# Optimization experiments

Measured on AMD Instinct MI355X. Metric: run time of the kernel, lower is better.

## Reference

```python
import jax, jax.numpy as jnp
import numpy as np
import math

TWO_PI = 2.0 * math.pi
B, K, DIM = 8, 1024, 4096
TEMP = 10.0  # softmax temperature from `sims * 10`


def setup_inputs() -> dict:
    key = jax.random.key(0)
    k1, k2 = jax.random.split(key)
    superposed = jax.random.uniform(k1, (B, DIM), jnp.float32, 0.0, TWO_PI)
    codebook = jax.random.uniform(k2, (K, DIM), jnp.float32, 0.0, TWO_PI)
    return {"superposed": superposed, "codebook": codebook, "num_iterations": 50}


def _cos_sim(est, codebook):
    # est: (B, dim), codebook: (K, dim) -> (B, K) mean cosine of phase diff
    return jnp.cos(est[:, None, :] - codebook[None, :, :]).mean(axis=-1)


def reference(superposed, codebook, num_iterations):
    # Batched resonator decode: iteratively refine estimate toward codebook
    # entries via softmax-weighted phasor superposition (torch.angle == atan2).
    cb_cos = jnp.cos(codebook)  # (K, dim) real part of codebook phasors
    cb_sin = jnp.sin(codebook)  # (K, dim) imag part

    def step(est, _):
        sims = _cos_sim(est, codebook)                 # (B, K)
        w = jax.nn.softmax(sims * TEMP, axis=-1)       # (B, K)
        re = w @ cb_cos                                # (B, dim)
        im = w @ cb_sin                                # (B, dim)
        est_new = jnp.arctan2(im, re) % TWO_PI         # angle of complex sum
        return est_new, None

    est, _ = jax.lax.scan(step, superposed, None, length=num_iterations)
    return _cos_sim(est, codebook)  # (B, K) final similarity scores
```

## Files before the change

### kernel.cpp

```cpp
#include <hip/hip_runtime.h>
#include <math.h>


#define KCODES 1024
#define DIMS   4096
#define BATCH  8
#define JROWS  (DIMS * 2)
#define NITER_MAX 50

#define T1_SZF  (JROWS * KCODES / 2)
#define T2_OFF  (T1_SZF)
#define T2_SZF  (T1_SZF)
#define EST_OFF (T2_OFF + T2_SZF)
#define EST_SZ  (JROWS * BATCH)
#define W_OFF   (EST_OFF + EST_SZ)

#define C2 (0.00244140625f * 1.4426950408889634f)

__device__ __forceinline__ ushort f2bf(float x) {
  unsigned u = __float_as_uint(x);
  return (ushort)((u + 0x7FFFu + ((u >> 16) & 1u)) >> 16);
}
__device__ __forceinline__ float bf2f(ushort u) {
  return __uint_as_float(((unsigned)u) << 16);
}

template <int CTRL>
__device__ __forceinline__ float dpp_add(float x) {
  int v = __builtin_amdgcn_update_dpp(0, __float_as_int(x), CTRL, 0xF, 0xF, false);
  return x + __int_as_float(v);
}
__device__ __forceinline__ float wave_sum64(float x) {
  x = dpp_add<0x111>(x);
  x = dpp_add<0x112>(x);
  x = dpp_add<0x114>(x);
  x = dpp_add<0x118>(x);
  x = dpp_add<0x142>(x);
  x = dpp_add<0x143>(x);
  return x;
}

__global__ __launch_bounds__(256) void k_trig(const float* __restrict__ cb,
                                              float* __restrict__ ws) {
  __shared__ float lc[64][65], ls[64][65];
  const int t  = threadIdx.x;
  const int bk = blockIdx.x & 15;
  const int bd = blockIdx.x >> 4;
  const int k0 = bk * 64, d0 = bd * 64;
  const int c = t & 63;
  #pragma unroll
  for (int i = 0; i < 16; ++i) {
    const int r = (t >> 6) + i * 4;
    float a = cb[(size_t)(k0 + r) * DIMS + d0 + c];
    float s, cc; sincosf(a, &s, &cc);
    lc[r][c] = cc; ls[r][c] = s;
  }
  __syncthreads();
  ushort* T1 = (ushort*)ws;
  #pragma unroll
  for (int j = 0; j < 16; ++j) {
    const int dd = (t >> 6) + j * 4;
    T1[(size_t)((d0 + dd) * 2 + 0) * KCODES + k0 + c] = f2bf(lc[c][dd]);
    T1[(size_t)((d0 + dd) * 2 + 1) * KCODES + k0 + c] = f2bf(ls[c][dd]);
  }
}

__global__ __launch_bounds__(256) void k_trig2(const float* __restrict__ cb,
                                               float* __restrict__ ws) {
  __shared__ float cbl[4][DIMS];
  const int t = threadIdx.x;
  const int g = blockIdx.x;
  #pragma unroll
  for (int c = 0; c < 4; ++c)
    #pragma unroll
    for (int q = 0; q < 4; ++q) {
      const int off = (q * 256 + t) * 4;
      *(float4*)&cbl[c][off] = *(const float4*)&cb[(size_t)(4 * g + c) * DIMS + off];
    }
  __syncthreads();

  ushort buf[128];
  #pragma unroll
  for (int dl = 0; dl < 16; ++dl) {
    #pragma unroll
    for (int c = 0; c < 4; ++c) {
      float s, cc; sincosf(cbl[c][16 * t + dl], &s, &cc);
      buf[(2 * dl + 0) * 4 + c] = f2bf(cc);
      buf[(2 * dl + 1) * 4 + c] = f2bf(s);
    }
  }
  uint4* dst = (uint4*)((ushort*)(ws + T2_OFF) + (size_t)g * (JROWS * 4) + t * 128);
  const uint4* src = (const uint4*)buf;
  #pragma unroll
  for (int i = 0; i < 16; ++i) dst[i] = src[i];
}

__global__ __launch_bounds__(256) void k_init(const float* __restrict__ sup,
                                              float* __restrict__ ws) {
  float* EST = ws + EST_OFF;
  const int i = blockIdx.x * 256 + threadIdx.x;
  const int b = i >> 12, d = i & 4095;
  float s, c; sincosf(sup[(size_t)b * DIMS + d], &s, &c);
  EST[(2 * d + 0) * BATCH + b] = c;
  EST[(2 * d + 1) * BATCH + b] = s;
}

__global__ __launch_bounds__(512) void k_simw(float* __restrict__ ws,
                                              const int* __restrict__ nit_p,
                                              float* __restrict__ out,
                                              int it) {
  const int NI = *nit_p;
  if (it > NI) return;
  const ushort* T2  = (const ushort*)(ws + T2_OFF);
  const float*  EST = ws + EST_OFF;
  float* W = ws + W_OFF;
  __shared__ float scr[8 * 32];

  const int t = threadIdx.x, lane = t & 63, wv = t >> 6;
  const int g = blockIdx.x;
  const ushort* trow = T2 + (size_t)g * (JROWS * 4);

  float acc[4][BATCH];
  #pragma unroll
  for (int c = 0; c < 4; ++c)
    #pragma unroll
    for (int b = 0; b < BATCH; ++b) acc[c][b] = 0.f;

  #pragma unroll 4
  for (int i = 0; i < 16; ++i) {
    const int j = i * 512 + t;
    const float4 e0 = *(const float4*)&EST[j * BATCH + 0];
    const float4 e1 = *(const float4*)&EST[j * BATCH + 4];
    const float ev[8] = {e0.x, e0.y, e0.z, e0.w, e1.x, e1.y, e1.z, e1.w};
    const ushort4 tu = *(const ushort4*)&trow[j * 4];
    const float tc[4] = {bf2f(tu.x), bf2f(tu.y), bf2f(tu.z), bf2f(tu.w)};
    #pragma unroll
    for (int c = 0; c < 4; ++c)
      #pragma unroll
      for (int b = 0; b < BATCH; ++b)
        acc[c][b] = fmaf(tc[c], ev[b], acc[c][b]);
  }

  #pragma unroll
  for (int c = 0; c < 4; ++c)
    #pragma unroll
    for (int b = 0; b < BATCH; ++b) {
      const float s = wave_sum64(acc[c][b]);
      if (lane == 63) scr[wv * 32 + c * BATCH + b] = s;
    }
  __syncthreads();

  if (t < 32) {
    float s = 0.f;
    #pragma unroll
    for (int w8 = 0; w8 < 8; ++w8) s += scr[w8 * 32 + t];
    const int c = t >> 3, b = t & 7;
    if (it == NI) out[b * KCODES + 4 * g + c] = s * (1.0f / (float)DIMS);
    else          W[b * KCODES + 4 * g + c] = exp2f(s * C2);
  }
}

__global__ __launch_bounds__(512) void k_est(float* __restrict__ ws,
                                             const int* __restrict__ nit_p,
                                             int it) {
  if (it >= *nit_p) return;
  const ushort* T1 = (const ushort*)ws;
  const float*  Wg = ws + W_OFF;
  float* EST = ws + EST_OFF;

  __shared__ float Wl[BATCH * KCODES];
  __shared__ float est_l[32 * BATCH];

  const int t = threadIdx.x, lane = t & 63, wv = t >> 6;
  const int r0 = blockIdx.x * 32;

  #pragma unroll
  for (int j = 0; j < 4; ++j) {
    const int idx = (j * 512 + t) * 4;
    *(float4*)&Wl[idx] = *(const float4*)&Wg[idx];
  }
  __syncthreads();

  const int rw = wv * 4;
  float acc[4][BATCH];
  #pragma unroll
  for (int r = 0; r < 4; ++r)
    #pragma unroll
    for (int b = 0; b < BATCH; ++b) acc[r][b] = 0.f;

  #pragma unroll
  for (int c = 0; c < 4; ++c) {
    const int kk = c * 256 + lane * 4;
    float4 wr[BATCH];
    #pragma unroll
    for (int b = 0; b < BATCH; ++b)
      wr[b] = *(const float4*)&Wl[b * KCODES + kk];
    #pragma unroll
    for (int r = 0; r < 4; ++r) {
      const ushort4 tu = *(const ushort4*)&T1[(size_t)(r0 + rw + r) * KCODES + kk];
      const float4 tv = make_float4(bf2f(tu.x), bf2f(tu.y), bf2f(tu.z), bf2f(tu.w));
      #pragma unroll
      for (int b = 0; b < BATCH; ++b) {
        acc[r][b] = fmaf(wr[b].x, tv.x, acc[r][b]);
        acc[r][b] = fmaf(wr[b].y, tv.y, acc[r][b]);
        acc[r][b] = fmaf(wr[b].z, tv.z, acc[r][b]);
        acc[r][b] = fmaf(wr[b].w, tv.w, acc[r][b]);
      }
    }
  }
  #pragma unroll
  for (int r = 0; r < 4; ++r)
    #pragma unroll
    for (int b = 0; b < BATCH; ++b) {
      const float s = wave_sum64(acc[r][b]);
      if (lane == 63) est_l[(rw + r) * BATCH + b] = s;
    }
  __syncthreads();

  if (t < 128) {
    const int dl = t >> 3, b = t & 7;
    const float re = est_l[(2 * dl + 0) * BATCH + b];
    const float im = est_l[(2 * dl + 1) * BATCH + b];
    const float n2 = fmaf(re, re, im * im);
    float ec, es;
    if (n2 > 0.f) {
      const float inv = rsqrtf(n2);
      ec = re * inv; es = im * inv;
    } else { ec = 1.f; es = 0.f; }
    est_l[(2 * dl + 0) * BATCH + b] = ec;
    est_l[(2 * dl + 1) * BATCH + b] = es;
  }
  __syncthreads();

  if (t < 256) EST[r0 * BATCH + t] = est_l[t];
}

extern "C" void kernel_launch(void* const* d_in, const int* in_sizes, int n_in,
                              void* d_out, int out_size, void* d_ws, size_t ws_size,
                              hipStream_t stream) {
  const float* sup = (const float*)d_in[0];
  const float* cbk = (const float*)d_in[1];
  const int*   nit = (const int*)d_in[2];
  float* outp = (float*)d_out;
  float* ws   = (float*)d_ws;

  hipLaunchKernelGGL(k_trig,  dim3(1024), dim3(256), 0, stream, cbk, ws);
  hipLaunchKernelGGL(k_trig2, dim3(256),  dim3(256), 0, stream, cbk, ws);
  hipLaunchKernelGGL(k_init,  dim3(128),  dim3(256), 0, stream, sup, ws);

  for (int it = 0; it < NITER_MAX; ++it) {
    hipLaunchKernelGGL(k_simw, dim3(256), dim3(512), 0, stream, ws, nit, outp, it);
    hipLaunchKernelGGL(k_est,  dim3(256), dim3(512), 0, stream, ws, nit, it);
  }
  hipLaunchKernelGGL(k_simw, dim3(256), dim3(512), 0, stream, ws, nit, outp, NITER_MAX);
}
```

Baseline: 765.3 us.

## Fuse similarity and estimate kernels into one launch per iteration with atomic flags

Merges the per-iteration similarity/softmax kernel and the estimate-update kernel into a single 512-block launch. The first 256 blocks compute weights and signal completion through hierarchical atomic counters. The remaining 256 blocks spin on a flag before reading the weights. This halves the kernel launch count and removes the inter-kernel gap. It relies on all 512 blocks being co-resident or being scheduled in order, and it adds a flag-buffer memset plus per-iteration weight buffers.

```diff
diff --git a/kernel.cpp b/kernel.cpp
--- a/kernel.cpp
+++ b/kernel.cpp
@@ -8,12 +8,20 @@
 #define JROWS  (DIMS * 2)
 #define NITER_MAX 50
 
-#define T1_SZF  (JROWS * KCODES / 2)
-#define T2_OFF  (T1_SZF)
-#define T2_SZF  (T1_SZF)
-#define EST_OFF (T2_OFF + T2_SZF)
-#define EST_SZ  (JROWS * BATCH)
-#define W_OFF   (EST_OFF + EST_SZ)
+#define T1_SZF   (JROWS * KCODES / 2)
+#define T2_OFF   (T1_SZF)
+#define T2_SZF   (T1_SZF)
+#define EST_OFF  (T2_OFF + T2_SZF)
+#define EST_SZ   (JROWS * BATCH)
+#define W_SZ     (BATCH * KCODES)
+#define WROT_OFF (EST_OFF + EST_SZ)
+#define WROT_SZ  (NITER_MAX * W_SZ)
+#define FLAG_OFF (WROT_OFF + WROT_SZ)
+
+#define NGRP    16
+#define GSTRIDE 16
+#define FGRP_SZ (NITER_MAX * NGRP * GSTRIDE)
+#define FFIN_SZ (NITER_MAX * GSTRIDE)
 
 #define C2 (0.00244140625f * 1.4426950408889634f)
 
@@ -105,134 +113,150 @@
   EST[(2 * d + 1) * BATCH + b] = s;
 }
 
-__global__ __launch_bounds__(512) void k_simw(float* __restrict__ ws,
+__global__ __launch_bounds__(512) void k_iter(float* __restrict__ ws,
                                               const int* __restrict__ nit_p,
                                               float* __restrict__ out,
                                               int it) {
   const int NI = *nit_p;
-  if (it > NI) return;
-  const ushort* T2  = (const ushort*)(ws + T2_OFF);
-  const float*  EST = ws + EST_OFF;
-  float* W = ws + W_OFF;
-  __shared__ float scr[8 * 32];
-
+  __shared__ float Wl[BATCH * KCODES];
+  float* W = ws + WROT_OFF + (size_t)it * W_SZ;
+  unsigned* fgrp = (unsigned*)(ws + FLAG_OFF);
+  unsigned* ffin = (unsigned*)(ws + FLAG_OFF) + FGRP_SZ;
   const int t = threadIdx.x, lane = t & 63, wv = t >> 6;
-  const int g = blockIdx.x;
-  const ushort* trow = T2 + (size_t)g * (JROWS * 4);
-
-  float acc[4][BATCH];
-  #pragma unroll
-  for (int c = 0; c < 4; ++c)
-    #pragma unroll
-    for (int b = 0; b < BATCH; ++b) acc[c][b] = 0.f;
-
-  #pragma unroll 4
-  for (int i = 0; i < 16; ++i) {
-    const int j = i * 512 + t;
-    const float4 e0 = *(const float4*)&EST[j * BATCH + 0];
-    const float4 e1 = *(const float4*)&EST[j * BATCH + 4];
-    const float ev[8] = {e0.x, e0.y, e0.z, e0.w, e1.x, e1.y, e1.z, e1.w};
-    const ushort4 tu = *(const ushort4*)&trow[j * 4];
-    const float tc[4] = {bf2f(tu.x), bf2f(tu.y), bf2f(tu.z), bf2f(tu.w)};
+  const int bid = blockIdx.x;
+
+  if (bid < 256) {
+    if (it > NI) return;
+    const ushort* T2  = (const ushort*)(ws + T2_OFF);
+    const float*  EST = ws + EST_OFF;
+    const int g = bid;
+    const ushort* trow = T2 + (size_t)g * (JROWS * 4);
+    float* scr = Wl;
+
+    float acc[4][BATCH];
     #pragma unroll
     for (int c = 0; c < 4; ++c)
       #pragma unroll
+      for (int b = 0; b < BATCH; ++b) acc[c][b] = 0.f;
+
+    #pragma unroll 4
+    for (int i = 0; i < 16; ++i) {
+      const int j = i * 512 + t;
+      const float4 e0 = *(const float4*)&EST[j * BATCH + 0];
+      const float4 e1 = *(const float4*)&EST[j * BATCH + 4];
+      const float ev[8] = {e0.x, e0.y, e0.z, e0.w, e1.x, e1.y, e1.z, e1.w};
+      const ushort4 tu = *(const ushort4*)&trow[j * 4];
+      const float tc[4] = {bf2f(tu.x), bf2f(tu.y), bf2f(tu.z), bf2f(tu.w)};
+      #pragma unroll
+      for (int c = 0; c < 4; ++c)
+        #pragma unroll
+        for (int b = 0; b < BATCH; ++b)
+          acc[c][b] = fmaf(tc[c], ev[b], acc[c][b]);
+    }
+
+    #pragma unroll
+    for (int c = 0; c < 4; ++c)
+      #pragma unroll
+      for (int b = 0; b < BATCH; ++b) {
+        const float s = wave_sum64(acc[c][b]);
+        if (lane == 63) scr[wv * 32 + c * BATCH + b] = s;
+      }
+    __syncthreads();
+
+    if (t < 32) {
+      float s = 0.f;
+      #pragma unroll
+      for (int w8 = 0; w8 < 8; ++w8) s += scr[w8 * 32 + t];
+      const int c = t >> 3, b = t & 7;
+      if (it == NI) out[b * KCODES + 4 * g + c] = s * (1.0f / (float)DIMS);
+      else          W[b * KCODES + 4 * g + c] = exp2f(s * C2);
+    }
+    if (it < NI) {
+      if (t < 64) __threadfence();
+      if (t == 0) {
+        unsigned* grp = fgrp + (it * NGRP + (bid & (NGRP - 1))) * GSTRIDE;
+        const unsigned old =
+            __hip_atomic_fetch_add(grp, 1u, __ATOMIC_RELEASE,
+                                   __HIP_MEMORY_SCOPE_AGENT);
+        if (old == 15u)
+          __hip_atomic_fetch_add(&ffin[it * GSTRIDE], 1u, __ATOMIC_RELEASE,
+                                 __HIP_MEMORY_SCOPE_AGENT);
+      }
+    }
+  } else {
+    if (it >= NI) return;
+    const ushort* T1 = (const ushort*)ws;
+    float* EST = ws + EST_OFF;
+    __shared__ float est_l[32 * BATCH];
+    const int r0 = (bid - 256) * 32;
+
+    if (t == 0) {
+      while (__hip_atomic_load(&ffin[it * GSTRIDE], __ATOMIC_RELAXED,
+                               __HIP_MEMORY_SCOPE_AGENT) < (unsigned)NGRP)
+        __builtin_amdgcn_s_sleep(1);
+    }
+    __syncthreads();
+
+    #pragma unroll
+    for (int j = 0; j < 4; ++j) {
+      const int idx = (j * 512 + t) * 4;
+      *(float4*)&Wl[idx] = *(const float4*)&W[idx];
+    }
+    __syncthreads();
+
+    const int rw = wv * 4;
+    float acc[4][BATCH];
+    #pragma unroll
+    for (int r = 0; r < 4; ++r)
+      #pragma unroll
+      for (int b = 0; b < BATCH; ++b) acc[r][b] = 0.f;
+
+    #pragma unroll
+    for (int c = 0; c < 4; ++c) {
+      const int kk = c * 256 + lane * 4;
+      float4 wr[BATCH];
+      #pragma unroll
       for (int b = 0; b < BATCH; ++b)
-        acc[c][b] = fmaf(tc[c], ev[b], acc[c][b]);
-  }
-
-  #pragma unroll
-  for (int c = 0; c < 4; ++c)
-    #pragma unroll
-    for (int b = 0; b < BATCH; ++b) {
-      const float s = wave_sum64(acc[c][b]);
-      if (lane == 63) scr[wv * 32 + c * BATCH + b] = s;
-    }
-  __syncthreads();
-
-  if (t < 32) {
-    float s = 0.f;
-    #pragma unroll
-    for (int w8 = 0; w8 < 8; ++w8) s += scr[w8 * 32 + t];
-    const int c = t >> 3, b = t & 7;
-    if (it == NI) out[b * KCODES + 4 * g + c] = s * (1.0f / (float)DIMS);
-    else          W[b * KCODES + 4 * g + c] = exp2f(s * C2);
-  }
-}
-
-__global__ __launch_bounds__(512) void k_est(float* __restrict__ ws,
-                                             const int* __restrict__ nit_p,
-                                             int it) {
-  if (it >= *nit_p) return;
-  const ushort* T1 = (const ushort*)ws;
-  const float*  Wg = ws + W_OFF;
-  float* EST = ws + EST_OFF;
-
-  __shared__ float Wl[BATCH * KCODES];
-  __shared__ float est_l[32 * BATCH];
-
-  const int t = threadIdx.x, lane = t & 63, wv = t >> 6;
-  const int r0 = blockIdx.x * 32;
-
-  #pragma unroll
-  for (int j = 0; j < 4; ++j) {
-    const int idx = (j * 512 + t) * 4;
-    *(float4*)&Wl[idx] = *(const float4*)&Wg[idx];
-  }
-  __syncthreads();
-
-  const int rw = wv * 4;
-  float acc[4][BATCH];
-  #pragma unroll
-  for (int r = 0; r < 4; ++r)
-    #pragma unroll
-    for (int b = 0; b < BATCH; ++b) acc[r][b] = 0.f;
-
-  #pragma unroll
-  for (int c = 0; c < 4; ++c) {
-    const int kk = c * 256 + lane * 4;
-    float4 wr[BATCH];
-    #pragma unroll
-    for (int b = 0; b < BATCH; ++b)
-      wr[b] = *(const float4*)&Wl[b * KCODES + kk];
-    #pragma unroll
-    for (int r = 0; r < 4; ++r) {
-      const ushort4 tu = *(const ushort4*)&T1[(size_t)(r0 + rw + r) * KCODES + kk];
-      const float4 tv = make_float4(bf2f(tu.x), bf2f(tu.y), bf2f(tu.z), bf2f(tu.w));
+        wr[b] = *(const float4*)&Wl[b * KCODES + kk];
+      #pragma unroll
+      for (int r = 0; r < 4; ++r) {
+        const ushort4 tu = *(const ushort4*)&T1[(size_t)(r0 + rw + r) * KCODES + kk];
+        const float4 tv = make_float4(bf2f(tu.x), bf2f(tu.y), bf2f(tu.z), bf2f(tu.w));
+        #pragma unroll
+        for (int b = 0; b < BATCH; ++b) {
+          acc[r][b] = fmaf(wr[b].x, tv.x, acc[r][b]);
+          acc[r][b] = fmaf(wr[b].y, tv.y, acc[r][b]);
+          acc[r][b] = fmaf(wr[b].z, tv.z, acc[r][b]);
+          acc[r][b] = fmaf(wr[b].w, tv.w, acc[r][b]);
+        }
+      }
+    }
+    #pragma unroll
+    for (int r = 0; r < 4; ++r)
       #pragma unroll
       for (int b = 0; b < BATCH; ++b) {
-        acc[r][b] = fmaf(wr[b].x, tv.x, acc[r][b]);
-        acc[r][b] = fmaf(wr[b].y, tv.y, acc[r][b]);
-        acc[r][b] = fmaf(wr[b].z, tv.z, acc[r][b]);
-        acc[r][b] = fmaf(wr[b].w, tv.w, acc[r][b]);
-      }
-    }
-  }
-  #pragma unroll
-  for (int r = 0; r < 4; ++r)
-    #pragma unroll
-    for (int b = 0; b < BATCH; ++b) {
-      const float s = wave_sum64(acc[r][b]);
-      if (lane == 63) est_l[(rw + r) * BATCH + b] = s;
-    }
-  __syncthreads();
-
-  if (t < 128) {
-    const int dl = t >> 3, b = t & 7;
-    const float re = est_l[(2 * dl + 0) * BATCH + b];
-    const float im = est_l[(2 * dl + 1) * BATCH + b];
-    const float n2 = fmaf(re, re, im * im);
-    float ec, es;
-    if (n2 > 0.f) {
-      const float inv = rsqrtf(n2);
-      ec = re * inv; es = im * inv;
-    } else { ec = 1.f; es = 0.f; }
-    est_l[(2 * dl + 0) * BATCH + b] = ec;
-    est_l[(2 * dl + 1) * BATCH + b] = es;
-  }
-  __syncthreads();
-
-  if (t < 256) EST[r0 * BATCH + t] = est_l[t];
+        const float s = wave_sum64(acc[r][b]);
+        if (lane == 63) est_l[(rw + r) * BATCH + b] = s;
+      }
+    __syncthreads();
+
+    if (t < 128) {
+      const int dl = t >> 3, b = t & 7;
+      const float re = est_l[(2 * dl + 0) * BATCH + b];
+      const float im = est_l[(2 * dl + 1) * BATCH + b];
+      const float n2 = fmaf(re, re, im * im);
+      float ec, es;
+      if (n2 > 0.f) {
+        const float inv = rsqrtf(n2);
+        ec = re * inv; es = im * inv;
+      } else { ec = 1.f; es = 0.f; }
+      est_l[(2 * dl + 0) * BATCH + b] = ec;
+      est_l[(2 * dl + 1) * BATCH + b] = es;
+    }
+    __syncthreads();
+
+    if (t < 256) EST[r0 * BATCH + t] = est_l[t];
+  }
 }
 
 extern "C" void kernel_launch(void* const* d_in, const int* in_sizes, int n_in,
@@ -244,13 +268,15 @@
   float* outp = (float*)d_out;
   float* ws   = (float*)d_ws;
 
+  hipMemsetAsync((char*)d_ws + (size_t)FLAG_OFF * sizeof(float), 0,
+                 (size_t)(FGRP_SZ + FFIN_SZ) * sizeof(unsigned), stream);
+
   hipLaunchKernelGGL(k_trig,  dim3(1024), dim3(256), 0, stream, cbk, ws);
   hipLaunchKernelGGL(k_trig2, dim3(256),  dim3(256), 0, stream, cbk, ws);
   hipLaunchKernelGGL(k_init,  dim3(128),  dim3(256), 0, stream, sup, ws);
 
-  for (int it = 0; it < NITER_MAX; ++it) {
-    hipLaunchKernelGGL(k_simw, dim3(256), dim3(512), 0, stream, ws, nit, outp, it);
-    hipLaunchKernelGGL(k_est,  dim3(256), dim3(512), 0, stream, ws, nit, it);
-  }
-  hipLaunchKernelGGL(k_simw, dim3(256), dim3(512), 0, stream, ws, nit, outp, NITER_MAX);
-}
+  for (int it = 0; it <= NITER_MAX; ++it) {
+    hipLaunchKernelGGL(k_iter, dim3(512), dim3(512), 0, stream,
+                       ws, nit, outp, it);
+  }
+}
```

Result: slower. 1.147 ms (+49.9%).
